# Kernel tuning notes

Measured on AMD Instinct MI355X. Metric: run time of the kernel, lower is better.

## Reference

```python
import jax, jax.numpy as jnp
import numpy as np

T, H, I, E, K = 2048, 1024, 768, 16, 4

def setup_inputs() -> dict:
    key = jax.random.key(0)
    k1, k2, k3, k4, k5 = jax.random.split(key, 5)
    hidden_states = jax.random.normal(k1, (T, H), dtype=jnp.float32)
    top_k_index = jax.random.randint(k2, (T, K), 0, E, dtype=jnp.int64)
    top_k_weights = jax.random.uniform(k3, (T, K), dtype=jnp.float32)
    gate_up_proj = jax.random.normal(k4, (E, 2 * I, H), dtype=jnp.float32) * 0.02
    down_proj = jax.random.normal(k5, (E, H, I), dtype=jnp.float32) * 0.02
    return {"hidden_states": hidden_states, "top_k_index": top_k_index,
            "top_k_weights": top_k_weights, "gate_up_proj": gate_up_proj,
            "down_proj": down_proj}

def reference(hidden_states, top_k_index, top_k_weights, gate_up_proj, down_proj):
    # Masked dense MoE: scan over experts, each expert does full-token GEMMs
    # and a per-token combine weight (sum of routing weights where routed to e).
    # index_add over token_idx == sum over k of (mask * weight) * expert_out.
    n_experts = gate_up_proj.shape[0]

    def body(acc, xs):
        w_gu, w_d, e = xs  # [2I,H], [H,I], scalar
        gu = hidden_states @ w_gu.T                 # [T, 2I]
        gate, up = jnp.split(gu, 2, axis=-1)        # [T, I] each
        h = jax.nn.silu(gate) * up                  # [T, I]
        out = h @ w_d.T                             # [T, H]
        w_tok = jnp.sum(jnp.where(top_k_index == e, top_k_weights, 0.0), axis=-1)  # [T]
        return acc + out * w_tok[:, None], None

    acc0 = jnp.zeros_like(hidden_states)
    final, _ = jax.lax.scan(body, acc0, (gate_up_proj, down_proj, jnp.arange(n_experts)))
    return final
```

## Files before the change

### kernel.cpp

```cpp
#include <hip/hip_runtime.h>
#include <hip/hip_bf16.h>
#include <stdint.h>

#define T_TOK 2048
#define H_DIM 1024
#define I_DIM 768
#define E_NUM 16
#define K_TOP 4
#define NSLOT (T_TOK * K_TOP)
#define PSLOT 10240
#define NTILE 80

typedef short  s16x8 __attribute__((ext_vector_type(8)));
typedef float  f32x4 __attribute__((ext_vector_type(4)));
typedef unsigned short u16x8 __attribute__((ext_vector_type(8)));
typedef unsigned int   u32x4 __attribute__((ext_vector_type(4)));

#define MEMFENCE asm volatile("" ::: "memory")

__device__ __forceinline__ void gload16(const void* g, void* l) {
  __builtin_amdgcn_global_load_lds(
      (const __attribute__((address_space(1))) uint32_t*)g,
      (__attribute__((address_space(3))) uint32_t*)l, 16, 0, 0);
}

__device__ __forceinline__ unsigned short f2bf(float f) {
  __hip_bfloat16 h = __float2bfloat16(f);
  return *reinterpret_cast<unsigned short*>(&h);
}

__device__ __forceinline__ unsigned int cvtpk(float lo, float hi) {
  unsigned int r;
  asm("v_cvt_pk_bf16_f32 %0, %1, %2" : "=v"(r) : "v"(lo), "v"(hi));
  return r;
}

__device__ __forceinline__ void write_b_row(char* bregion, int r, int half,
                                            f32x4 f0, f32x4 f1, f32x4 f2, f32x4 f3) {
  union { u32x4 u; u16x8 s; } a_, b_;
  a_.u[0] = cvtpk(f0[0], f0[1]); a_.u[1] = cvtpk(f0[2], f0[3]);
  a_.u[2] = cvtpk(f1[0], f1[1]); a_.u[3] = cvtpk(f1[2], f1[3]);
  b_.u[0] = cvtpk(f2[0], f2[1]); b_.u[1] = cvtpk(f2[2], f2[3]);
  b_.u[2] = cvtpk(f3[0], f3[1]); b_.u[3] = cvtpk(f3[2], f3[3]);
  int xr = (r >> 1) & 3;
  char* wb = bregion + r * 64;
  *(u16x8*)(wb + (((2*half + 0) ^ xr) * 16)) = a_.s;
  *(u16x8*)(wb + (((2*half + 1) ^ xr) * 16)) = b_.s;
}

__global__ __launch_bounds__(256) void cvt_bf16_kernel(
    const float* __restrict__ in, unsigned short* __restrict__ out, int n8) {
  int i = blockIdx.x * 256 + threadIdx.x;
  if (i >= n8) return;
  const float4* p = (const float4*)in;
  float4 a = p[2 * (size_t)i];
  float4 b = p[2 * (size_t)i + 1];
  u16x8 o;
  o[0] = f2bf(a.x); o[1] = f2bf(a.y); o[2] = f2bf(a.z); o[3] = f2bf(a.w);
  o[4] = f2bf(b.x); o[5] = f2bf(b.y); o[6] = f2bf(b.z); o[7] = f2bf(b.w);
  *(u16x8*)(out + (size_t)i * 8) = o;
}

__global__ __launch_bounds__(256) void route_kernel(
    const int* __restrict__ idx, const float* __restrict__ wts,
    int* __restrict__ slot_tok, float* __restrict__ slot_w,
    int* __restrict__ slot_of, int* __restrict__ tile_expert) {
  __shared__ int cnt[256][16];
  __shared__ int tot[16];
  __shared__ int pb[17];
  int tid = threadIdx.x;

  for (int e = 0; e < 16; ++e) cnt[tid][e] = 0;
  const int s0 = tid * 32;
  for (int i = 0; i < 32; ++i) {
    int e = idx[s0 + i] & 15;
    cnt[tid][e]++;
  }
  __syncthreads();
  if (tid < 16) {
    int run = 0;
    for (int c = 0; c < 256; ++c) { int v = cnt[c][tid]; cnt[c][tid] = run; run += v; }
    tot[tid] = run;
  }
  __syncthreads();
  if (tid == 0) {
    int acc = 0;
    for (int e = 0; e < 16; ++e) { pb[e] = acc; acc += (tot[e] + 127) & ~127; }
    pb[16] = acc;
  }
  __syncthreads();
  for (int p = tid; p < PSLOT; p += 256) { slot_tok[p] = 0; slot_w[p] = 0.0f; }
  if (tid < NTILE) {
    int ef = -1;
    for (int e = 0; e < 16; ++e)
      if (tid * 128 >= pb[e] && tid * 128 < pb[e + 1]) ef = e;
    tile_expert[tid] = ef;
  }
  __syncthreads();
  for (int i = 0; i < 32; ++i) {
    int s = s0 + i;
    int e = idx[s] & 15;
    int pos = pb[e] + cnt[tid][e]++;
    slot_tok[pos] = s >> 2;
    slot_w[pos]   = wts[s];
    slot_of[s]    = pos;
  }
}

__global__ __launch_bounds__(512) void gemm1_kernel(
    const unsigned short* __restrict__ Xbf,
    const float* __restrict__ Wgu,
    const int* __restrict__ slot_tok,
    const int* __restrict__ tile_expert,
    unsigned short* __restrict__ hbuf) {
  int bid  = blockIdx.y * 6 + blockIdx.x;
  int sbid = (bid & 7) * 60 + (bid >> 3);
  int by   = sbid / 6;
  int bx   = sbid % 6;
  int e = tile_expert[by];
  if (e < 0) return;
  int m0 = by * 128;
  int t = threadIdx.x;
  int lane = t & 63, w = t >> 6;
  int wr = w >> 2, wc = w & 3;
  int l15 = lane & 15, lhi = lane >> 4;

  __shared__ char lds[2 * 40960];
  char* buf0 = lds;
  char* buf1 = lds + 40960;

  int tokA = slot_tok[m0 + (t >> 2)];
  int aswz = ((t & 3) ^ ((t >> 3) & 3)) * 16;
  const char* gA = (const char*)(Xbf + (size_t)tokA * H_DIM) + aswz;

  const char* gBs[4];
#pragma unroll
  for (int c = 0; c < 4; ++c) {
    int r = c * 64 + (t >> 3);
    int grow = e * 1536 + ((r < 128) ? (bx * 128 + r) : (768 + bx * 128 + (r - 128)));
    int q = (t & 7) ^ (r & 7);
    gBs[c] = (const char*)(Wgu + (size_t)grow * H_DIM) + q * 16;
  }

  int pswz = (lhi ^ ((l15 >> 1) & 3)) * 8;

  f32x4 accg[4][2] = {};
  f32x4 accu[4][2] = {};

#define NT1 32
#define G1_STAGE(bufp, kt) do {                               \
    size_t ao = (size_t)(kt) * 64;                            \
    size_t bo = (size_t)(kt) * 128;                           \
    gload16(gA + ao, (bufp) + t * 16);                        \
    gload16(gBs[0] + bo, (bufp) + 8192 + t * 16);             \
    gload16(gBs[1] + bo, (bufp) + 16384 + t * 16);            \
    gload16(gBs[2] + bo, (bufp) + 24576 + t * 16);            \
    gload16(gBs[3] + bo, (bufp) + 32768 + t * 16);            \
  } while (0)

#define B_FRAG(dst, cb, rb) do {                                              \
    const char* base_ = (cb) + 8192 + (rb) * 128;                             \
    f32x4 x0_ = *(const f32x4*)(base_ + (((2*lhi    ) ^ ((rb) & 7)) * 16));   \
    f32x4 x1_ = *(const f32x4*)(base_ + (((2*lhi + 1) ^ ((rb) & 7)) * 16));   \
    union { u32x4 u; s16x8 s; } pk_;                                          \
    pk_.u[0] = cvtpk(x0_[0], x0_[1]);                                         \
    pk_.u[1] = cvtpk(x0_[2], x0_[3]);                                         \
    pk_.u[2] = cvtpk(x1_[0], x1_[1]);                                         \
    pk_.u[3] = cvtpk(x1_[2], x1_[3]);                                         \
    dst = pk_.s;                                                              \
  } while (0)

#define G1_COMPUTE(cb) do {                                                            \
    const short* La = (const short*)(cb);                                              \
    s16x8 af[4], bg[2], bu[2];                                                         \
    _Pragma("unroll")                                                                  \
    for (int mi = 0; mi < 4; ++mi)                                                     \
      af[mi] = *(const s16x8*)(La + (wr * 64 + mi * 16 + l15) * 32 + pswz);            \
    _Pragma("unroll")                                                                  \
    for (int ni = 0; ni < 2; ++ni) {                                                   \
      int rbg = wc * 32 + ni * 16 + l15;                                               \
      B_FRAG(bg[ni], (cb), rbg);                                                       \
      B_FRAG(bu[ni], (cb), rbg + 128);                                                 \
    }                                                                                  \
    __builtin_amdgcn_s_setprio(1);                                                     \
    _Pragma("unroll")                                                                  \
    for (int mi = 0; mi < 4; ++mi)                                                     \
      _Pragma("unroll")                                                                \
      for (int ni = 0; ni < 2; ++ni) {                                                 \
        accg[mi][ni] = __builtin_amdgcn_mfma_f32_16x16x32_bf16(af[mi], bg[ni], accg[mi][ni], 0, 0, 0); \
        accu[mi][ni] = __builtin_amdgcn_mfma_f32_16x16x32_bf16(af[mi], bu[ni], accu[mi][ni], 0, 0, 0); \
      }                                                                                \
    __builtin_amdgcn_s_setprio(0);                                                     \
  } while (0)

  G1_STAGE(buf0, 0);
  int cur = 0;
  for (int kt = 0; kt < NT1; ++kt) {
    char* cbuf = cur ? buf1 : buf0;
    char* nbuf = cur ? buf0 : buf1;
    if (kt + 1 < NT1) {
      MEMFENCE;
      G1_STAGE(nbuf, kt + 1);
      asm volatile("s_waitcnt vmcnt(5)" ::: "memory");
    } else {
      asm volatile("s_waitcnt vmcnt(0)" ::: "memory");
    }
    __builtin_amdgcn_s_barrier();
    MEMFENCE;
    G1_COMPUTE(cbuf);
    MEMFENCE;
    __builtin_amdgcn_s_barrier();
    cur ^= 1;
  }
#undef G1_STAGE
#undef G1_COMPUTE
#undef B_FRAG

#pragma unroll
  for (int mi = 0; mi < 4; ++mi) {
#pragma unroll
    for (int ni = 0; ni < 2; ++ni) {
      int col = bx * 128 + wc * 32 + ni * 16 + l15;
#pragma unroll
      for (int q = 0; q < 4; ++q) {
        int m = m0 + wr * 64 + mi * 16 + lhi * 4 + q;
        float g = accg[mi][ni][q];
        float u = accu[mi][ni][q];
        float s = g / (1.0f + __expf(-g));
        hbuf[(size_t)m * I_DIM + col] = f2bf(s * u);
      }
    }
  }
}

__global__ __launch_bounds__(256) void gemm2_kernel(
    const unsigned short* __restrict__ hbuf,
    const float* __restrict__ Wd,
    const int* __restrict__ slot_tok,
    const float* __restrict__ slot_w,
    const int* __restrict__ tile_expert,
    float* __restrict__ y) {
  int bid  = blockIdx.y * 8 + blockIdx.x;
  int sbid = (bid & 7) * 80 + (bid >> 3);
  int by   = sbid >> 3;
  int bx   = sbid & 7;
  int e = tile_expert[by];
  if (e < 0) return;
  int m0 = by * 128;
  int tid = threadIdx.x;
  int lane = tid & 63, w = tid >> 6;
  int wr = w >> 1, wc = w & 1;

  __shared__ short lds[2 * 8192];
  char* buf0 = (char*)lds;
  char* buf1 = buf0 + 16384;

  int srow = tid >> 2;
  int swzc = ((tid & 3) ^ ((tid >> 3) & 3)) * 16;
  const char* gA0 = (const char*)(hbuf + (size_t)(m0 + srow) * I_DIM) + swzc;
  const char* gA1 = (const char*)(hbuf + (size_t)(m0 + 64 + srow) * I_DIM) + swzc;

  int brow = tid >> 1;
  int half = tid & 1;
  const float* gB = Wd + ((size_t)e * 1024 + bx * 128 + brow) * I_DIM + half * 16;

  int pswz = ((lane >> 4) ^ (((lane & 15) >> 1) & 3)) * 8;

  f32x4 acc[4][4] = {};
  f32x4 s0_0, s0_1, s0_2, s0_3, s1_0, s1_1, s1_2, s1_3;
  f32x4 s2_0, s2_1, s2_2, s2_3, s3_0, s3_1, s3_2, s3_3;

#define NT2 24
#define A_GLOAD2(kt, bufp) do {                               \
    int kk_ = (kt) < NT2 ? (kt) : NT2 - 1;                    \
    int ko_ = kk_ * 64;                                       \
    gload16(gA0 + ko_, (bufp) + tid * 16);                    \
    gload16(gA1 + ko_, (bufp) + 4096 + tid * 16);             \
  } while (0)
#define B_LOAD2(v0, v1, v2, v3, kt) do {                      \
    int kk_ = (kt) < NT2 ? (kt) : NT2 - 1;                    \
    const f32x4* p_ = (const f32x4*)(gB + (size_t)kk_ * 32);  \
    v0 = p_[0]; v1 = p_[1]; v2 = p_[2]; v3 = p_[3];           \
  } while (0)

#define G2_COMPUTE(bufp) do {                                                          \
    const short* La = (const short*)(bufp);                                            \
    s16x8 af[4], bf[4];                                                                \
    _Pragma("unroll")                                                                  \
    for (int mi = 0; mi < 4; ++mi)                                                     \
      af[mi] = *(const s16x8*)(La + (wr * 64 + mi * 16 + (lane & 15)) * 32 + pswz);    \
    _Pragma("unroll")                                                                  \
    for (int ni = 0; ni < 4; ++ni)                                                     \
      bf[ni] = *(const s16x8*)(La + 4096 + (wc * 64 + ni * 16 + (lane & 15)) * 32 + pswz); \
    _Pragma("unroll")                                                                  \
    for (int mi = 0; mi < 4; ++mi)                                                     \
      _Pragma("unroll")                                                                \
      for (int ni = 0; ni < 4; ++ni)                                                   \
        acc[mi][ni] = __builtin_amdgcn_mfma_f32_16x16x32_bf16(af[mi], bf[ni], acc[mi][ni], 0, 0, 0); \
  } while (0)

#define ITER2(kt, wv0, wv1, wv2, wv3, lv0, lv1, lv2, lv3) do {  \
    char* cbuf_ = ((kt) & 1) ? buf1 : buf0;                     \
    char* nbuf_ = ((kt) & 1) ? buf0 : buf1;                     \
    MEMFENCE;                                                   \
    A_GLOAD2((kt) + 1, nbuf_);                                  \
    MEMFENCE;                                                   \
    B_LOAD2(lv0, lv1, lv2, lv3, (kt) + 3);                      \
    asm volatile("s_waitcnt vmcnt(10)" ::: "memory");           \
    write_b_row(nbuf_ + 8192, brow, half, wv0, wv1, wv2, wv3);  \
    asm volatile("s_waitcnt lgkmcnt(0)" ::: "memory");          \
    __builtin_amdgcn_s_barrier();                               \
    MEMFENCE;                                                   \
    G2_COMPUTE(cbuf_);                                          \
    MEMFENCE;                                                   \
    __builtin_amdgcn_s_barrier();                               \
  } while (0)

  A_GLOAD2(0, buf0);
  MEMFENCE;
  B_LOAD2(s0_0, s0_1, s0_2, s0_3, 0);
  MEMFENCE;
  B_LOAD2(s1_0, s1_1, s1_2, s1_3, 1);
  MEMFENCE;
  B_LOAD2(s2_0, s2_1, s2_2, s2_3, 2);
  asm volatile("s_waitcnt vmcnt(8)" ::: "memory");
  write_b_row(buf0 + 8192, brow, half, s0_0, s0_1, s0_2, s0_3);

  for (int kt = 0; kt < NT2; kt += 4) {
    ITER2(kt + 0, s1_0, s1_1, s1_2, s1_3, s3_0, s3_1, s3_2, s3_3);
    ITER2(kt + 1, s2_0, s2_1, s2_2, s2_3, s0_0, s0_1, s0_2, s0_3);
    ITER2(kt + 2, s3_0, s3_1, s3_2, s3_3, s1_0, s1_1, s1_2, s1_3);
    ITER2(kt + 3, s0_0, s0_1, s0_2, s0_3, s2_0, s2_1, s2_2, s2_3);
  }
#undef ITER2
#undef G2_COMPUTE
#undef B_LOAD2
#undef A_GLOAD2

#pragma unroll
  for (int mi = 0; mi < 4; ++mi) {
#pragma unroll
    for (int q = 0; q < 4; ++q) {
      int m = m0 + wr * 64 + mi * 16 + (lane >> 4) * 4 + q;
      float wgt = slot_w[m];
      float* orow = y + (size_t)m * H_DIM + bx * 128 + wc * 64 + (lane & 15);
#pragma unroll
      for (int ni = 0; ni < 4; ++ni)
        orow[ni * 16] = acc[mi][ni][q] * wgt;
    }
  }
}

__global__ __launch_bounds__(256) void combine_kernel(
    const float* __restrict__ y, const int* __restrict__ slot_of,
    float* __restrict__ out) {
  int t = blockIdx.x;
  int c = threadIdx.x * 4;
  int s0 = slot_of[t * 4 + 0], s1 = slot_of[t * 4 + 1];
  int s2 = slot_of[t * 4 + 2], s3 = slot_of[t * 4 + 3];
  f32x4 v0 = *(const f32x4*)(y + (size_t)s0 * H_DIM + c);
  f32x4 v1 = *(const f32x4*)(y + (size_t)s1 * H_DIM + c);
  f32x4 v2 = *(const f32x4*)(y + (size_t)s2 * H_DIM + c);
  f32x4 v3 = *(const f32x4*)(y + (size_t)s3 * H_DIM + c);
  f32x4 r = (v0 + v1) + (v2 + v3);
  *(f32x4*)(out + (size_t)t * H_DIM + c) = r;
}

extern "C" void kernel_launch(void* const* d_in, const int* in_sizes, int n_in,
                              void* d_out, int out_size, void* d_ws, size_t ws_size,
                              hipStream_t stream) {
  const float* hs       = (const float*)d_in[0];
  const int*   topk_idx = (const int*)d_in[1];
  const float* topk_w   = (const float*)d_in[2];
  const float* w_gu     = (const float*)d_in[3];
  const float* w_d      = (const float*)d_in[4];
  float* out = (float*)d_out;

  char* ws = (char*)d_ws;
  unsigned short* Xbf  = (unsigned short*)(ws);
  unsigned short* hbuf = (unsigned short*)(ws + 4194304);
  float*          y    = (float*)(ws + 19922944);
  int*   slot_tok    = (int*)(ws + 61865984);
  float* slot_w      = (float*)(ws + 61906944);
  int*   slot_of     = (int*)(ws + 61947904);
  int*   tile_expert = (int*)(ws + 61980672);

  cvt_bf16_kernel<<<1024, 256, 0, stream>>>(hs, Xbf, T_TOK * H_DIM / 8);
  route_kernel<<<1, 256, 0, stream>>>(topk_idx, topk_w, slot_tok, slot_w,
                                      slot_of, tile_expert);

  gemm1_kernel<<<dim3(6, NTILE), 512, 0, stream>>>(Xbf, w_gu, slot_tok, tile_expert, hbuf);
  gemm2_kernel<<<dim3(8, NTILE), 256, 0, stream>>>(hbuf, w_d, slot_tok, slot_w, tile_expert, y);
  combine_kernel<<<T_TOK, 256, 0, stream>>>(y, slot_of, out);
}
```

Measured before the change: 133.0 us.

## Pre-convert gate/up weights to bf16 and restructure gemm1 to 4-wave tiles

Adds a separate conversion kernel that turns the full fp32 gate_up weight tensor into bf16 in workspace, so gemm1 loads bf16 B tiles directly instead of converting fp32 fragments inside the inner loop. gemm1 drops to 256 threads with larger per-wave tiles (4x4 accumulators for gate and up) and a smaller LDS footprint. The aim is to halve the B traffic that gemm1 streams through LDS and to remove the per-fragment conversion ALU work. The cost is an extra pass over 100MB of fp32 weights on every call, and the y buffer now aliases the Wgubf region.

```diff
diff --git a/kernel.cpp b/kernel.cpp
--- a/kernel.cpp
+++ b/kernel.cpp
@@ -107,9 +107,9 @@
   }
 }
 
-__global__ __launch_bounds__(512) void gemm1_kernel(
+__global__ __launch_bounds__(256) void gemm1_kernel(
     const unsigned short* __restrict__ Xbf,
-    const float* __restrict__ Wgu,
+    const unsigned short* __restrict__ Wgubf,
     const int* __restrict__ slot_tok,
     const int* __restrict__ tile_expert,
     unsigned short* __restrict__ hbuf) {
@@ -122,74 +122,70 @@
   int m0 = by * 128;
   int t = threadIdx.x;
   int lane = t & 63, w = t >> 6;
-  int wr = w >> 2, wc = w & 3;
+  int wr = w >> 1, wc = w & 1;
   int l15 = lane & 15, lhi = lane >> 4;
 
-  __shared__ char lds[2 * 40960];
+  __shared__ char lds[2 * 24576];
   char* buf0 = lds;
-  char* buf1 = lds + 40960;
-
-  int tokA = slot_tok[m0 + (t >> 2)];
-  int aswz = ((t & 3) ^ ((t >> 3) & 3)) * 16;
-  const char* gA = (const char*)(Xbf + (size_t)tokA * H_DIM) + aswz;
+  char* buf1 = lds + 24576;
+
+  int srow = t >> 2;
+  int swz  = ((t & 3) ^ ((t >> 3) & 3)) * 16;
+
+  int tok0 = slot_tok[m0 + srow];
+  int tok1 = slot_tok[m0 + 64 + srow];
+  const char* gA0 = (const char*)(Xbf + (size_t)tok0 * H_DIM) + swz;
+  const char* gA1 = (const char*)(Xbf + (size_t)tok1 * H_DIM) + swz;
 
   const char* gBs[4];
 #pragma unroll
   for (int c = 0; c < 4; ++c) {
-    int r = c * 64 + (t >> 3);
+    int r = c * 64 + srow;
     int grow = e * 1536 + ((r < 128) ? (bx * 128 + r) : (768 + bx * 128 + (r - 128)));
-    int q = (t & 7) ^ (r & 7);
-    gBs[c] = (const char*)(Wgu + (size_t)grow * H_DIM) + q * 16;
+    gBs[c] = (const char*)(Wgubf + (size_t)grow * H_DIM) + swz;
   }
 
   int pswz = (lhi ^ ((l15 >> 1) & 3)) * 8;
 
-  f32x4 accg[4][2] = {};
-  f32x4 accu[4][2] = {};
+  f32x4 accg[4][4] = {};
+  f32x4 accu[4][4] = {};
 
 #define NT1 32
 #define G1_STAGE(bufp, kt) do {                               \
-    size_t ao = (size_t)(kt) * 64;                            \
-    size_t bo = (size_t)(kt) * 128;                           \
-    gload16(gA + ao, (bufp) + t * 16);                        \
-    gload16(gBs[0] + bo, (bufp) + 8192 + t * 16);             \
-    gload16(gBs[1] + bo, (bufp) + 16384 + t * 16);            \
-    gload16(gBs[2] + bo, (bufp) + 24576 + t * 16);            \
-    gload16(gBs[3] + bo, (bufp) + 32768 + t * 16);            \
-  } while (0)
-
-#define B_FRAG(dst, cb, rb) do {                                              \
-    const char* base_ = (cb) + 8192 + (rb) * 128;                             \
-    f32x4 x0_ = *(const f32x4*)(base_ + (((2*lhi    ) ^ ((rb) & 7)) * 16));   \
-    f32x4 x1_ = *(const f32x4*)(base_ + (((2*lhi + 1) ^ ((rb) & 7)) * 16));   \
-    union { u32x4 u; s16x8 s; } pk_;                                          \
-    pk_.u[0] = cvtpk(x0_[0], x0_[1]);                                         \
-    pk_.u[1] = cvtpk(x0_[2], x0_[3]);                                         \
-    pk_.u[2] = cvtpk(x1_[0], x1_[1]);                                         \
-    pk_.u[3] = cvtpk(x1_[2], x1_[3]);                                         \
-    dst = pk_.s;                                                              \
+    size_t ko = (size_t)(kt) * 64;                            \
+    gload16(gA0 + ko, (bufp) + t * 16);                       \
+    gload16(gA1 + ko, (bufp) + 4096 + t * 16);                \
+    gload16(gBs[0] + ko, (bufp) + 8192 + t * 16);             \
+    gload16(gBs[1] + ko, (bufp) + 12288 + t * 16);            \
+    gload16(gBs[2] + ko, (bufp) + 16384 + t * 16);            \
+    gload16(gBs[3] + ko, (bufp) + 20480 + t * 16);            \
   } while (0)
 
 #define G1_COMPUTE(cb) do {                                                            \
     const short* La = (const short*)(cb);                                              \
-    s16x8 af[4], bg[2], bu[2];                                                         \
+    s16x8 af[4], bfr[4];                                                               \
     _Pragma("unroll")                                                                  \
     for (int mi = 0; mi < 4; ++mi)                                                     \
       af[mi] = *(const s16x8*)(La + (wr * 64 + mi * 16 + l15) * 32 + pswz);            \
     _Pragma("unroll")                                                                  \
-    for (int ni = 0; ni < 2; ++ni) {                                                   \
-      int rbg = wc * 32 + ni * 16 + l15;                                               \
-      B_FRAG(bg[ni], (cb), rbg);                                                       \
-      B_FRAG(bu[ni], (cb), rbg + 128);                                                 \
-    }                                                                                  \
+    for (int ni = 0; ni < 4; ++ni)                                                     \
+      bfr[ni] = *(const s16x8*)(La + 4096 + (wc * 64 + ni * 16 + l15) * 32 + pswz);    \
     __builtin_amdgcn_s_setprio(1);                                                     \
     _Pragma("unroll")                                                                  \
     for (int mi = 0; mi < 4; ++mi)                                                     \
       _Pragma("unroll")                                                                \
-      for (int ni = 0; ni < 2; ++ni) {                                                 \
-        accg[mi][ni] = __builtin_amdgcn_mfma_f32_16x16x32_bf16(af[mi], bg[ni], accg[mi][ni], 0, 0, 0); \
-        accu[mi][ni] = __builtin_amdgcn_mfma_f32_16x16x32_bf16(af[mi], bu[ni], accu[mi][ni], 0, 0, 0); \
-      }                                                                                \
+      for (int ni = 0; ni < 4; ++ni)                                                   \
+        accg[mi][ni] = __builtin_amdgcn_mfma_f32_16x16x32_bf16(af[mi], bfr[ni], accg[mi][ni], 0, 0, 0); \
+    __builtin_amdgcn_s_setprio(0);                                                     \
+    _Pragma("unroll")                                                                  \
+    for (int ni = 0; ni < 4; ++ni)                                                     \
+      bfr[ni] = *(const s16x8*)(La + 4096 + (128 + wc * 64 + ni * 16 + l15) * 32 + pswz); \
+    __builtin_amdgcn_s_setprio(1);                                                     \
+    _Pragma("unroll")                                                                  \
+    for (int mi = 0; mi < 4; ++mi)                                                     \
+      _Pragma("unroll")                                                                \
+      for (int ni = 0; ni < 4; ++ni)                                                   \
+        accu[mi][ni] = __builtin_amdgcn_mfma_f32_16x16x32_bf16(af[mi], bfr[ni], accu[mi][ni], 0, 0, 0); \
     __builtin_amdgcn_s_setprio(0);                                                     \
   } while (0)
 
@@ -201,7 +197,7 @@
     if (kt + 1 < NT1) {
       MEMFENCE;
       G1_STAGE(nbuf, kt + 1);
-      asm volatile("s_waitcnt vmcnt(5)" ::: "memory");
+      asm volatile("s_waitcnt vmcnt(6)" ::: "memory");
     } else {
       asm volatile("s_waitcnt vmcnt(0)" ::: "memory");
     }
@@ -214,13 +210,12 @@
   }
 #undef G1_STAGE
 #undef G1_COMPUTE
-#undef B_FRAG
 
 #pragma unroll
   for (int mi = 0; mi < 4; ++mi) {
 #pragma unroll
-    for (int ni = 0; ni < 2; ++ni) {
-      int col = bx * 128 + wc * 32 + ni * 16 + l15;
+    for (int ni = 0; ni < 4; ++ni) {
+      int col = bx * 128 + wc * 64 + ni * 16 + l15;
 #pragma unroll
       for (int q = 0; q < 4; ++q) {
         int m = m0 + wr * 64 + mi * 16 + lhi * 4 + q;
@@ -377,19 +372,21 @@
   float* out = (float*)d_out;
 
   char* ws = (char*)d_ws;
-  unsigned short* Xbf  = (unsigned short*)(ws);
-  unsigned short* hbuf = (unsigned short*)(ws + 4194304);
-  float*          y    = (float*)(ws + 19922944);
-  int*   slot_tok    = (int*)(ws + 61865984);
-  float* slot_w      = (float*)(ws + 61906944);
-  int*   slot_of     = (int*)(ws + 61947904);
-  int*   tile_expert = (int*)(ws + 61980672);
-
-  cvt_bf16_kernel<<<1024, 256, 0, stream>>>(hs, Xbf, T_TOK * H_DIM / 8);
+  unsigned short* Xbf   = (unsigned short*)(ws);
+  unsigned short* Wgubf = (unsigned short*)(ws + 4194304);
+  float*          y     = (float*)(ws + 4194304);
+  unsigned short* hbuf  = (unsigned short*)(ws + 54525952);
+  int*   slot_tok    = (int*)(ws + 70254592);
+  float* slot_w      = (float*)(ws + 70295552);
+  int*   slot_of     = (int*)(ws + 70336512);
+  int*   tile_expert = (int*)(ws + 70369280);
+
+  cvt_bf16_kernel<<<1024,  256, 0, stream>>>(hs,   Xbf,   T_TOK * H_DIM / 8);
+  cvt_bf16_kernel<<<12288, 256, 0, stream>>>(w_gu, Wgubf, E_NUM * 2 * I_DIM * H_DIM / 8);
   route_kernel<<<1, 256, 0, stream>>>(topk_idx, topk_w, slot_tok, slot_w,
                                       slot_of, tile_expert);
 
-  gemm1_kernel<<<dim3(6, NTILE), 512, 0, stream>>>(Xbf, w_gu, slot_tok, tile_expert, hbuf);
+  gemm1_kernel<<<dim3(6, NTILE), 256, 0, stream>>>(Xbf, Wgubf, slot_tok, tile_expert, hbuf);
   gemm2_kernel<<<dim3(8, NTILE), 256, 0, stream>>>(hbuf, w_d, slot_tok, slot_w, tile_expert, y);
   combine_kernel<<<T_TOK, 256, 0, stream>>>(y, slot_of, out);
 }
```

Result: no change. 135.5 us (+1.9%).
